# Optimization experiments

Hardware: AMD Instinct MI355X
Metric: run time of the kernel (lower is better)

Reference implementation:

```python
import jax, jax.numpy as jnp
import numpy as np

INPUT_DIM = 400
G_DIM = 3 * INPUT_DIM          # 1200, per-mention repr dim
GIJ_DIM = 9 * INPUT_DIM        # 3600, pair repr dim
HIDDEN = 150
M = 10000                      # candidate mentions
P = 2000                       # pruned mentions


def _pair_positions(P, K):
    """Static (numpy) construction of (i_pos, j_pos) into pruned_idx, matching
    the original double loop: for idx, for j in pruned_idx[max(0, idx-K):idx]."""
    I = np.repeat(np.arange(P)[:, None], K, axis=1)      # [P, K]
    Jpos = I - np.arange(K, 0, -1)[None, :]              # j = idx-K .. idx-1 (ascending)
    valid = Jpos >= 0
    return I[valid], Jpos[valid]                         # row-major => same ordering as loop


def setup_inputs() -> dict:
    key = jax.random.key(0)
    ks = jax.random.split(key, 8)
    mention_reprs = jax.random.normal(ks[0], (M, G_DIM), dtype=jnp.float32)
    pruned_idx = jnp.sort(jax.random.randint(ks[1], (P,), 0, M))
    s = 0.02
    return {
        "mention_reprs": mention_reprs,
        "pruned_idx": pruned_idx,
        "K": 50,
        "W1": jax.random.normal(ks[2], (GIJ_DIM, HIDDEN), dtype=jnp.float32) * s,
        "b1": jnp.zeros((HIDDEN,), dtype=jnp.float32),
        "W2": jax.random.normal(ks[3], (HIDDEN, HIDDEN), dtype=jnp.float32) * s,
        "b2": jnp.zeros((HIDDEN,), dtype=jnp.float32),
        "W3": jax.random.normal(ks[4], (HIDDEN, 1), dtype=jnp.float32) * s,
        "b3": jnp.zeros((1,), dtype=jnp.float32),
    }


def reference(mention_reprs, pruned_idx, K, W1, b1, W2, b2, W3, b3):
    P_ = pruned_idx.shape[0]
    i_pos, j_pos = _pair_positions(P_, int(K))           # static shapes
    g_i = mention_reprs[pruned_idx[i_pos]]               # [NP, G_DIM]
    g_j = mention_reprs[pruned_idx[j_pos]]               # [NP, G_DIM]
    pairwise = jnp.concatenate([g_i, g_j, g_i * g_j], axis=1)  # [NP, 9*input_dim]
    h = jax.nn.relu(pairwise @ W1 + b1)
    h = jax.nn.relu(h @ W2 + b2)
    return (h @ W3 + b3).squeeze(-1)                     # [NP]
```

## Files before the change

kernel.cpp:

```cpp
#include <hip/hip_runtime.h>


typedef __attribute__((ext_vector_type(8))) short short8;
typedef __attribute__((ext_vector_type(4))) float f32x4;

constexpr int DP    = 1216;
constexpr int HPAD  = 160;
constexpr int NKC   = 38;
constexpr int NKC2  = 5;
constexpr int WCHU  = 10240;
constexpr int WCH1  = 5120;
constexpr int ROWS  = 128;
constexpr int KD    = 50;
constexpr int TI    = 5;
constexpr int PB    = TI * KD;
constexpr int NGR   = KD + TI;
constexpr int TD    = KD * (KD - 1) / 2;

__device__ __forceinline__ ushort bf16_rne(float x) {
  uint u = __float_as_uint(x);
  u += 0x7FFFu + ((u >> 16) & 1u);
  return (ushort)(u >> 16);
}
__device__ __forceinline__ float bf16f(ushort h) {
  return __uint_as_float((uint)h << 16);
}
__device__ __forceinline__ f32x4 mfma16(short8 a, short8 b, f32x4 c) {
  return __builtin_amdgcn_mfma_f32_16x16x32_bf16(a, b, c, 0, 0, 0);
}
__device__ __forceinline__ void g2lds16(const void* g, void* l) {
  __builtin_amdgcn_global_load_lds(
      (const __attribute__((address_space(1))) void*)g,
      (__attribute__((address_space(3))) void*)l, 16, 0, 0);
}
__device__ __forceinline__ void stage_hi(const ushort* gs, ushort* lb,
                                         int w, int lane) {
  const char* g = (const char*)gs + w * 1024 + lane * 16;
  char* l = (char*)lb + w * 1024;
  g2lds16(g, l);
  g2lds16(g + 4096, l + 4096);
  if (w < 2) g2lds16(g + 8192, l + 8192);
}
__device__ __forceinline__ void stage_chunk(const ushort* gsrc, ushort* lbuf,
                                            int w, int lane) {
  const char* g = (const char*)gsrc + w * 5120 + lane * 16;
  char* l = (char*)lbuf + w * 5120;
#pragma unroll
  for (int q = 0; q < 5; ++q) g2lds16(g + q * 1024, l + q * 1024);
}
__device__ __forceinline__ void stage_G5(const float* __restrict__ G, int b0,
                                         int c, float* buf, int w, int lane) {
#pragma unroll
  for (int r = 0; r < 2; ++r) {
    const int slot = r * 256 + w * 64 + lane;
    int row = slot >> 3, grp = slot & 7;
    row = min(row, NGR - 1);
    const float* src =
        G + (size_t)(b0 + row) * DP + c * 32 + ((grp ^ (row & 7)) << 2);
    char* dst = (char*)buf + (r * 256 + w * 64) * 16;
    g2lds16(src, dst);
  }
}
__device__ __forceinline__ short8 mulcvt8(float4 a0, float4 a1, float4 b0,
                                          float4 b1) {
  float p[8] = {a0.x * b0.x, a0.y * b0.y, a0.z * b0.z, a0.w * b0.w,
                a1.x * b1.x, a1.y * b1.y, a1.z * b1.z, a1.w * b1.w};
  uint r[4];
#pragma unroll
  for (int e = 0; e < 4; ++e) {
    uint u0 = __float_as_uint(p[2 * e]);
    uint u1 = __float_as_uint(p[2 * e + 1]);
    u0 += 0x7FFFu + ((u0 >> 16) & 1u);
    u1 += 0x7FFFu + ((u1 >> 16) & 1u);
    r[e] = __builtin_amdgcn_perm(u1, u0, 0x07060302u);
  }
  uint4 h = make_uint4(r[0], r[1], r[2], r[3]);
  return *(short8*)&h;
}
__device__ __forceinline__ void split1(const float* a, short8& hi, short8& lo) {
  const float4 a0 = *(const float4*)a, a1 = *(const float4*)(a + 4);
  float p[8] = {a0.x, a0.y, a0.z, a0.w, a1.x, a1.y, a1.z, a1.w};
  uint h[4], l[4];
#pragma unroll
  for (int e = 0; e < 4; ++e) {
    uint u0 = __float_as_uint(p[2 * e]), u1 = __float_as_uint(p[2 * e + 1]);
    float r0 = p[2 * e] - __uint_as_float(u0 & 0xffff0000u);
    float r1 = p[2 * e + 1] - __uint_as_float(u1 & 0xffff0000u);
    h[e] = __builtin_amdgcn_perm(u1, u0, 0x07060302u);
    l[e] = __builtin_amdgcn_perm(__float_as_uint(r1), __float_as_uint(r0),
                                 0x07060302u);
  }
  uint4 hu = make_uint4(h[0], h[1], h[2], h[3]);
  uint4 lu = make_uint4(l[0], l[1], l[2], l[3]);
  hi = *(short8*)&hu; lo = *(short8*)&lu;
}
__device__ __forceinline__ void pair_ij(int r, int K, int NP, int& i, int& j) {
  if (r >= NP) { i = 1; j = 0; return; }
  const int T = K * (K - 1) / 2;
  if (r < T) {
    int ii = (int)((1.0f + sqrtf(1.0f + 8.0f * (float)r)) * 0.5f);
    while (ii * (ii - 1) / 2 > r) --ii;
    while ((ii + 1) * ii / 2 <= r) ++ii;
    i = ii; j = r - ii * (ii - 1) / 2;
  } else {
    const int rp = r - T, q = rp / K;
    i = K + q; j = i - K + (rp - q * K);
  }
}

__global__ void k_prep_gather(const float* __restrict__ W1,
                              const float* __restrict__ W2,
                              const float* __restrict__ M,
                              const int* __restrict__ pidx,
                              ushort* __restrict__ W1ab,
                              ushort* __restrict__ W1c_hi,
                              ushort* __restrict__ W2_hi,
                              float* __restrict__ G, int P) {
  if ((int)blockIdx.x < P) {
    const int i = blockIdx.x;
    const int r = pidx[i];
    const float4* src = reinterpret_cast<const float4*>(M + (size_t)r * 1200);
    float4* dst = reinterpret_cast<float4*>(G + (size_t)i * DP);
    for (int t = threadIdx.x; t < DP / 4; t += blockDim.x)
      dst[t] = (t < 300) ? src[t] : make_float4(0.f, 0.f, 0.f, 0.f);
    return;
  }
  const int NAB = 2 * NKC * HPAD * 32;
  const int NC = NKC * HPAD * 32;
  int idx = (blockIdx.x - P) * 256 + threadIdx.x;
  if (idx < NAB) {
    int s = idx / NC, r1 = idx % NC;
    int c = r1 / (HPAD * 32), r2 = r1 % (HPAD * 32);
    int col = r2 >> 5, kk = r2 & 31;
    int k = c * 32 + kk;
    float v = (k < 1200 && col < 150) ? W1[((size_t)s * 1200 + k) * 150 + col] : 0.f;
    ushort h = bf16_rne(v);
    ushort l = bf16_rne(v - bf16f(h));
    size_t base = (size_t)(s * NKC + c) * WCHU;
    int i0 = (col * 32 + kk) ^ ((col & 7) << 3);
    W1ab[base + i0] = h;
    W1ab[base + i0 + 5120] = l;
  } else if (idx < NAB + NC) {
    int r1 = idx - NAB;
    int c = r1 / (HPAD * 32), r2 = r1 % (HPAD * 32);
    int col = r2 >> 5, kk = r2 & 31;
    int k = c * 32 + kk;
    float v = (k < 1200 && col < 150)
                  ? W1[((size_t)2 * 1200 + k) * 150 + col] : 0.f;
    int i0 = (col * 32 + kk) ^ ((col & 7) << 3);
    W1c_hi[(size_t)c * WCH1 + i0] = bf16_rne(v);
  } else {
    int r1 = idx - NAB - NC;
    if (r1 < NKC2 * HPAD * 32) {
      int c = r1 / (HPAD * 32), r2 = r1 % (HPAD * 32);
      int col = r2 >> 5, kk = r2 & 31;
      int k = c * 32 + kk;
      float v = (k < 150 && col < 150) ? W2[(size_t)k * 150 + col] : 0.f;
      int i0 = (col * 32 + kk) ^ ((col & 7) << 3);
      W2_hi[(size_t)c * WCH1 + i0] = bf16_rne(v);
    }
  }
}

__global__ __launch_bounds__(256, 4) void k_precomp(
    const float* __restrict__ G, const ushort* __restrict__ W1ab,
    const float* __restrict__ b1, float* __restrict__ AB, int P) {
  __shared__ __align__(16) ushort Wb[2][WCHU];
  const int tid = threadIdx.x, lane = tid & 63, w = tid >> 6;
  const int l15 = lane & 15, kb = lane >> 4;
  const int rt = w & 1, ch = w >> 1;
  const int r0 = blockIdx.x * 32;
  const int slab = blockIdx.y;
  const ushort* wsrc = W1ab + (size_t)slab * NKC * WCHU;

  const int row = min(r0 + rt * 16 + l15, P - 1);
  const float* g = G + (size_t)row * DP + kb * 8;
  const int lbase = (l15 * 32 + kb * 8) ^ ((l15 & 7) << 3);

  f32x4 acc[5];
#pragma unroll
  for (int b = 0; b < 5; ++b) acc[b] = (f32x4)(0.f);

  stage_chunk(wsrc, Wb[0], w, lane);
  short8 ah, al;
  split1(g, ah, al);

  for (int c = 0; c < NKC; ++c) {
    __syncthreads();
    if (c < NKC - 1)
      stage_chunk(wsrc + (size_t)(c + 1) * WCHU, Wb[(c + 1) & 1], w, lane);
    const ushort* wb = Wb[c & 1];
#pragma unroll
    for (int ct = 0; ct < 5; ++ct) {
      const int ob = (ch * 5 + ct) * 512 + lbase;
      const short8 bh = *(const short8*)&wb[ob];
      const short8 bl = *(const short8*)&wb[ob + 5120];
      acc[ct] = mfma16(ah, bh, acc[ct]);
      acc[ct] = mfma16(al, bh, acc[ct]);
      acc[ct] = mfma16(ah, bl, acc[ct]);
    }
    if (c < NKC - 1) split1(g + (c + 1) * 32, ah, al);
  }
  float* outp = AB + (size_t)slab * P * HPAD;
#pragma unroll
  for (int q = 0; q < 4; ++q) {
    const int r = r0 + rt * 16 + kb * 4 + q;
    if (r < P) {
#pragma unroll
      for (int ct = 0; ct < 5; ++ct) {
        const int col = (ch * 5 + ct) * 16 + l15;
        float v = acc[ct][q];
        if (slab == 0 && col < 150) v += b1[col];
        outp[(size_t)r * HPAD + col] = v;
      }
    }
  }
}

__global__ __launch_bounds__(256, 2) void k_pair(
    const float* __restrict__ G, const ushort* __restrict__ W1c_hi,
    const float* __restrict__ AB, ushort* __restrict__ H1,
    int P, int K, int NP, int ND, int wmax) {
  __shared__ __align__(16) ushort Wb[2][WCH1];
  __shared__ __align__(16) float Gs[2][2048];
  __shared__ int tI[ROWS], tJ[ROWS];
  const int tid = threadIdx.x, lane = tid & 63, w = tid >> 6;
  const int l15 = lane & 15, kb = lane >> 4;
  const int lswz = (l15 * 32 + kb * 8) ^ ((l15 & 7) << 3);

  if ((int)blockIdx.x < ND) {
    const int q8 = ND >> 3, r8 = ND & 7;
    const int xcd = blockIdx.x & 7, sidx = blockIdx.x >> 3;
    const int bid = (xcd < r8) ? xcd * (q8 + 1) + sidx
                               : r8 * (q8 + 1) + (xcd - r8) * q8 + sidx;
    const int i0 = KD + bid * TI;
    const int b0 = i0 - KD;

    int sI0[4], sI1[4], sJ0[4], sJ1[4];
#pragma unroll
    for (int rt = 0; rt < 4; ++rt) {
      const int q = min(w * 64 + rt * 16 + l15, PB - 1);
      const int li = KD + q / KD, lj = q / KD + q % KD;
      sI0[rt] = li * 8 + ((2 * kb) ^ (li & 7));
      sI1[rt] = li * 8 + ((2 * kb + 1) ^ (li & 7));
      sJ0[rt] = lj * 8 + ((2 * kb) ^ (lj & 7));
      sJ1[rt] = lj * 8 + ((2 * kb + 1) ^ (lj & 7));
    }

    f32x4 acc[4][10];
#pragma unroll
    for (int a = 0; a < 4; ++a)
#pragma unroll
      for (int b = 0; b < 10; ++b) acc[a][b] = (f32x4)(0.f);

    stage_G5(G, b0, 0, Gs[0], w, lane);
    stage_hi(W1c_hi, Wb[0], w, lane);
    __syncthreads();

#pragma unroll 2
    for (int c = 0; c < NKC; ++c) {
      if (c) __syncthreads();
      if (c < NKC - 1) {
        stage_G5(G, b0, c + 1, Gs[(c + 1) & 1], w, lane);
        stage_hi(W1c_hi + (size_t)(c + 1) * WCH1, Wb[(c + 1) & 1], w, lane);
      }
      const float4* gp = (const float4*)Gs[c & 1];
      const ushort* wb = Wb[c & 1];
      short8 a[4];
#pragma unroll
      for (int rt = 0; rt < 4; ++rt)
        a[rt] = mulcvt8(gp[sI0[rt]], gp[sI1[rt]], gp[sJ0[rt]], gp[sJ1[rt]]);
#pragma unroll
      for (int ct = 0; ct < 10; ++ct) {
        const short8 bh = *(const short8*)&wb[ct * 512 + lswz];
        acc[0][ct] = mfma16(a[0], bh, acc[0][ct]);
        acc[1][ct] = mfma16(a[1], bh, acc[1][ct]);
        acc[2][ct] = mfma16(a[2], bh, acc[2][ct]);
        acc[3][ct] = mfma16(a[3], bh, acc[3][ct]);
      }
    }

#pragma unroll
    for (int rt = 0; rt < 4; ++rt)
#pragma unroll
      for (int qq = 0; qq < 4; ++qq) {
        const int rr = w * 64 + rt * 16 + kb * 4 + qq;
        if (rr < PB) {
          const int ii = i0 + rr / KD;
          const int jj = ii - KD + rr % KD;
          const float* Ar = AB + (size_t)ii * HPAD;
          const float* Br = AB + ((size_t)P + jj) * HPAD;
          ushort* hrow = H1 + (size_t)(TD + bid * PB + rr) * HPAD;
#pragma unroll
          for (int ct = 0; ct < 10; ++ct) {
            const int col = ct * 16 + l15;
            const float v = acc[rt][ct][qq] + Ar[col] + Br[col];
            hrow[col] = bf16_rne(fmaxf(v, 0.f));
          }
        }
      }
  } else {
    const int r0 = ((int)blockIdx.x - ND) * ROWS;
    if (tid < ROWS) {
      int i, j;
      pair_ij(r0 + tid, K, NP, i, j);
      tI[tid] = i; tJ[tid] = j;
    }
    stage_hi(W1c_hi, Wb[0], w, lane);
    __syncthreads();

    const int rowA = w * 32 + l15, rowB = rowA + 16;
    const float* gi0 = G + (size_t)tI[rowA] * DP + kb * 8;
    const float* gj0 = G + (size_t)tJ[rowA] * DP + kb * 8;
    const float* gi1 = G + (size_t)tI[rowB] * DP + kb * 8;
    const float* gj1 = G + (size_t)tJ[rowB] * DP + kb * 8;

    f32x4 acc[2][10];
#pragma unroll
    for (int a = 0; a < 2; ++a)
#pragma unroll
      for (int b = 0; b < 10; ++b) acc[a][b] = (f32x4)(0.f);

    float4 x00 = *(const float4*)gi0, x01 = *(const float4*)(gi0 + 4);
    float4 y00 = *(const float4*)gj0, y01 = *(const float4*)(gj0 + 4);
    float4 x10 = *(const float4*)gi1, x11 = *(const float4*)(gi1 + 4);
    float4 y10 = *(const float4*)gj1, y11 = *(const float4*)(gj1 + 4);

#pragma unroll 2
    for (int c = 0; c < NKC; ++c) {
      if (c) __syncthreads();
      if (c < NKC - 1)
        stage_hi(W1c_hi + (size_t)(c + 1) * WCH1, Wb[(c + 1) & 1], w, lane);
      const short8 a0 = mulcvt8(x00, x01, y00, y01);
      const short8 a1 = mulcvt8(x10, x11, y10, y11);
      if (c < NKC - 1) {
        const int cn = c + 1;
        x00 = *(const float4*)(gi0 + cn * 32); x01 = *(const float4*)(gi0 + cn * 32 + 4);
        y00 = *(const float4*)(gj0 + cn * 32); y01 = *(const float4*)(gj0 + cn * 32 + 4);
        x10 = *(const float4*)(gi1 + cn * 32); x11 = *(const float4*)(gi1 + cn * 32 + 4);
        y10 = *(const float4*)(gj1 + cn * 32); y11 = *(const float4*)(gj1 + cn * 32 + 4);
      }
      const ushort* wb = Wb[c & 1];
#pragma unroll
      for (int ct = 0; ct < 10; ++ct) {
        const short8 bh = *(const short8*)&wb[ct * 512 + lswz];
        acc[0][ct] = mfma16(a0, bh, acc[0][ct]);
        acc[1][ct] = mfma16(a1, bh, acc[1][ct]);
      }
    }

#pragma unroll
    for (int rt = 0; rt < 2; ++rt)
#pragma unroll
      for (int q = 0; q < 4; ++q) {
        const int rr = w * 32 + rt * 16 + kb * 4 + q;
        const int gr = r0 + rr;
        if (gr < wmax) {
          const float* Ar = AB + (size_t)tI[rr] * HPAD;
          const float* Br = AB + ((size_t)P + tJ[rr]) * HPAD;
          ushort* hrow = H1 + (size_t)gr * HPAD;
#pragma unroll
          for (int ct = 0; ct < 10; ++ct) {
            const int col = ct * 16 + l15;
            const float v = acc[rt][ct][q] + Ar[col] + Br[col];
            hrow[col] = bf16_rne(fmaxf(v, 0.f));
          }
        }
      }
  }
}

__global__ __launch_bounds__(256, 3) void k_mlp(
    const ushort* __restrict__ H1, const ushort* __restrict__ W2_hi,
    const float* __restrict__ b2, const float* __restrict__ W3,
    const float* __restrict__ b3, float* __restrict__ out, int NP) {
  __shared__ __align__(16) ushort Wb[2][WCH1];
  const int tid = threadIdx.x, lane = tid & 63, w = tid >> 6;
  const int l15 = lane & 15, kb = lane >> 4;
  const int r0 = blockIdx.x * ROWS;
  const int lswz = (l15 * 32 + kb * 8) ^ ((l15 & 7) << 3);

  const ushort* h0 = H1 + (size_t)(r0 + w * 32 + l15) * HPAD + kb * 8;
  const ushort* h1 = H1 + (size_t)(r0 + w * 32 + 16 + l15) * HPAD + kb * 8;

  f32x4 acc[2][10];
#pragma unroll
  for (int a = 0; a < 2; ++a)
#pragma unroll
    for (int b = 0; b < 10; ++b) acc[a][b] = (f32x4)(0.f);

  stage_hi(W2_hi, Wb[0], w, lane);
  short8 a0 = *(const short8*)h0;
  short8 a1 = *(const short8*)h1;

#pragma unroll
  for (int c = 0; c < NKC2; ++c) {
    __syncthreads();
    if (c < NKC2 - 1)
      stage_hi(W2_hi + (size_t)(c + 1) * WCH1, Wb[(c + 1) & 1], w, lane);
    const ushort* wb = Wb[c & 1];
#pragma unroll
    for (int ct = 0; ct < 10; ++ct) {
      const short8 bh = *(const short8*)&wb[ct * 512 + lswz];
      acc[0][ct] = mfma16(a0, bh, acc[0][ct]);
      acc[1][ct] = mfma16(a1, bh, acc[1][ct]);
    }
    if (c < NKC2 - 1) {
      a0 = *(const short8*)(h0 + (c + 1) * 32);
      a1 = *(const short8*)(h1 + (c + 1) * 32);
    }
  }
  const float b3v = b3[0];
#pragma unroll
  for (int rt = 0; rt < 2; ++rt)
#pragma unroll
    for (int q = 0; q < 4; ++q) {
      float s = 0.f;
#pragma unroll
      for (int ct = 0; ct < 10; ++ct) {
        const int col = ct * 16 + l15;
        const float b2c = (col < 150) ? b2[col] : 0.f;
        const float w3c = (col < 150) ? W3[col] : 0.f;
        s = fmaf(fmaxf(acc[rt][ct][q] + b2c, 0.f), w3c, s);
      }
      s += __shfl_xor(s, 1); s += __shfl_xor(s, 2);
      s += __shfl_xor(s, 4); s += __shfl_xor(s, 8);
      if (l15 == 0) {
        const int gr = r0 + w * 32 + rt * 16 + kb * 4 + q;
        if (gr < NP) out[gr] = s + b3v;
      }
    }
}

extern "C" void kernel_launch(void* const* d_in, const int* in_sizes, int n_in,
                              void* d_out, int out_size, void* d_ws, size_t ws_size,
                              hipStream_t stream) {
  const float* M    = (const float*)d_in[0];
  const int*   pidx = (const int*)d_in[1];
  const float* W1   = (const float*)d_in[3];
  const float* b1   = (const float*)d_in[4];
  const float* W2   = (const float*)d_in[5];
  const float* b2   = (const float*)d_in[6];
  const float* W3   = (const float*)d_in[7];
  const float* b3   = (const float*)d_in[8];
  float* out = (float*)d_out;

  const int P = in_sizes[1];
  const int NP = out_size;
  int K = 50;
  for (int k = 1; k <= P; ++k) {
    const long long np = (long long)k * (k - 1) / 2 + (long long)(P - k) * k;
    if (np == (long long)NP) { K = k; break; }
  }
  const int nb = (NP + ROWS - 1) / ROWS;

  float* G = (float*)d_ws;
  float* AB = G + (size_t)P * DP;
  ushort* W1ab = (ushort*)(AB + (size_t)2 * P * HPAD);
  ushort* W1c_hi = W1ab + (size_t)2 * NKC * WCHU;
  ushort* W2_hi = W1c_hi + (size_t)NKC * WCH1;
  ushort* H1 = W2_hi + (size_t)NKC2 * WCH1;

  const int prepN = (2 * NKC + NKC + NKC2) * HPAD * 32;
  const int prepB = (prepN + 255) / 256;
  k_prep_gather<<<P + prepB, 256, 0, stream>>>(W1, W2, M, pidx, W1ab, W1c_hi,
                                               W2_hi, G, P);
  dim3 gp((P + 31) / 32, 2);
  k_precomp<<<gp, 256, 0, stream>>>(G, W1ab, b1, AB, P);

  int ND = 0, wmax = NP;
  if (K == KD && P > KD && (P - KD) % TI == 0) {
    ND = (P - KD) / TI;
    wmax = TD;
  }
  const int genB = (wmax + ROWS - 1) / ROWS;
  k_pair<<<ND + genB, 256, 0, stream>>>(G, W1c_hi, AB, H1, P, K, NP, ND, wmax);
  k_mlp<<<nb, 256, 0, stream>>>(H1, W2_hi, b2, W3, b3, out, NP);
}
```

Measured before the change: 125.9 us.

## Retile pair kernel to 8 anchors per 512-thread block with per-wave i reuse

The dense pair path now handles 8 anchor mentions per block using 8 waves, one per anchor, so each wave loads its g_i row once and reuses it across all 64 j rows. Per-block G staging shrinks to one 16-byte load per thread and W1 staging is split across more waves. The generic fallback path is reorganized into head and tail regions so it can cover pairs left over when P-K is not divisible by 8. The bf16 conversion in the product helper now uses the HIP bf16x2 intrinsic. Doubling the block size raises register pressure under the new launch bounds and may reduce occupancy.

```diff
diff --git a/kernel.cpp b/kernel.cpp
--- a/kernel.cpp
+++ b/kernel.cpp
@@ -1,4 +1,5 @@
 #include <hip/hip_runtime.h>
+#include <hip/hip_bf16.h>
 
 
 typedef __attribute__((ext_vector_type(8))) short short8;
@@ -12,9 +13,8 @@
 constexpr int WCH1  = 5120;
 constexpr int ROWS  = 128;
 constexpr int KD    = 50;
-constexpr int TI    = 5;
-constexpr int PB    = TI * KD;
-constexpr int NGR   = KD + TI;
+constexpr int TI8   = 8;
+constexpr int NGR8  = KD + TI8;
 constexpr int TD    = KD * (KD - 1) / 2;
 
 __device__ __forceinline__ ushort bf16_rne(float x) {
@@ -41,6 +41,13 @@
   g2lds16(g + 4096, l + 4096);
   if (w < 2) g2lds16(g + 8192, l + 8192);
 }
+__device__ __forceinline__ void stage_hi8(const ushort* gs, ushort* lb,
+                                          int w, int lane) {
+  const char* g = (const char*)gs + w * 1024 + lane * 16;
+  char* l = (char*)lb + w * 1024;
+  g2lds16(g, l);
+  if (w < 2) g2lds16(g + 8192, l + 8192);
+}
 __device__ __forceinline__ void stage_chunk(const ushort* gsrc, ushort* lbuf,
                                             int w, int lane) {
   const char* g = (const char*)gsrc + w * 5120 + lane * 16;
@@ -48,18 +55,13 @@
 #pragma unroll
   for (int q = 0; q < 5; ++q) g2lds16(g + q * 1024, l + q * 1024);
 }
-__device__ __forceinline__ void stage_G5(const float* __restrict__ G, int b0,
+__device__ __forceinline__ void stage_G8(const float* __restrict__ G, int b0,
                                          int c, float* buf, int w, int lane) {
-#pragma unroll
-  for (int r = 0; r < 2; ++r) {
-    const int slot = r * 256 + w * 64 + lane;
-    int row = slot >> 3, grp = slot & 7;
-    row = min(row, NGR - 1);
-    const float* src =
-        G + (size_t)(b0 + row) * DP + c * 32 + ((grp ^ (row & 7)) << 2);
-    char* dst = (char*)buf + (r * 256 + w * 64) * 16;
-    g2lds16(src, dst);
-  }
+  const int slot = w * 64 + lane;
+  const int row = min(slot >> 3, NGR8 - 1), grp = slot & 7;
+  const float* src =
+      G + (size_t)(b0 + row) * DP + c * 32 + ((grp ^ (row & 7)) << 2);
+  g2lds16(src, (char*)buf + w * 1024);
 }
 __device__ __forceinline__ short8 mulcvt8(float4 a0, float4 a1, float4 b0,
                                           float4 b1) {
@@ -68,11 +70,8 @@
   uint r[4];
 #pragma unroll
   for (int e = 0; e < 4; ++e) {
-    uint u0 = __float_as_uint(p[2 * e]);
-    uint u1 = __float_as_uint(p[2 * e + 1]);
-    u0 += 0x7FFFu + ((u0 >> 16) & 1u);
-    u1 += 0x7FFFu + ((u1 >> 16) & 1u);
-    r[e] = __builtin_amdgcn_perm(u1, u0, 0x07060302u);
+    __hip_bfloat162 t = __float22bfloat162_rn(make_float2(p[2 * e], p[2 * e + 1]));
+    r[e] = *(uint*)&t;
   }
   uint4 h = make_uint4(r[0], r[1], r[2], r[3]);
   return *(short8*)&h;
@@ -217,13 +216,13 @@
   }
 }
 
-__global__ __launch_bounds__(256, 2) void k_pair(
+__global__ __launch_bounds__(512, 2) void k_pair(
     const float* __restrict__ G, const ushort* __restrict__ W1c_hi,
     const float* __restrict__ AB, ushort* __restrict__ H1,
-    int P, int K, int NP, int ND, int wmax) {
+    int P, int K, int NP, int ND, int headB, int tail0, int wlimHead) {
   __shared__ __align__(16) ushort Wb[2][WCH1];
   __shared__ __align__(16) float Gs[2][2048];
-  __shared__ int tI[ROWS], tJ[ROWS];
+  __shared__ int tI[256], tJ[256];
   const int tid = threadIdx.x, lane = tid & 63, w = tid >> 6;
   const int l15 = lane & 15, kb = lane >> 4;
   const int lswz = (l15 * 32 + kb * 8) ^ ((l15 & 7) << 3);
@@ -233,18 +232,18 @@
     const int xcd = blockIdx.x & 7, sidx = blockIdx.x >> 3;
     const int bid = (xcd < r8) ? xcd * (q8 + 1) + sidx
                                : r8 * (q8 + 1) + (xcd - r8) * q8 + sidx;
-    const int i0 = KD + bid * TI;
+    const int i0 = KD + bid * TI8;
     const int b0 = i0 - KD;
 
-    int sI0[4], sI1[4], sJ0[4], sJ1[4];
+    const int gir = KD + w;
+    const int sI0 = gir * 8 + ((2 * kb) ^ (gir & 7));
+    const int sI1 = gir * 8 + ((2 * kb + 1) ^ (gir & 7));
+    int sJ0[4], sJ1[4];
 #pragma unroll
     for (int rt = 0; rt < 4; ++rt) {
-      const int q = min(w * 64 + rt * 16 + l15, PB - 1);
-      const int li = KD + q / KD, lj = q / KD + q % KD;
-      sI0[rt] = li * 8 + ((2 * kb) ^ (li & 7));
-      sI1[rt] = li * 8 + ((2 * kb + 1) ^ (li & 7));
-      sJ0[rt] = lj * 8 + ((2 * kb) ^ (lj & 7));
-      sJ1[rt] = lj * 8 + ((2 * kb + 1) ^ (lj & 7));
+      const int rj = min(w + rt * 16 + l15, NGR8 - 1);
+      sJ0[rt] = rj * 8 + ((2 * kb) ^ (rj & 7));
+      sJ1[rt] = rj * 8 + ((2 * kb + 1) ^ (rj & 7));
     }
 
     f32x4 acc[4][10];
@@ -253,23 +252,24 @@
 #pragma unroll
       for (int b = 0; b < 10; ++b) acc[a][b] = (f32x4)(0.f);
 
-    stage_G5(G, b0, 0, Gs[0], w, lane);
-    stage_hi(W1c_hi, Wb[0], w, lane);
+    stage_G8(G, b0, 0, Gs[0], w, lane);
+    stage_hi8(W1c_hi, Wb[0], w, lane);
     __syncthreads();
 
 #pragma unroll 2
     for (int c = 0; c < NKC; ++c) {
       if (c) __syncthreads();
       if (c < NKC - 1) {
-        stage_G5(G, b0, c + 1, Gs[(c + 1) & 1], w, lane);
-        stage_hi(W1c_hi + (size_t)(c + 1) * WCH1, Wb[(c + 1) & 1], w, lane);
+        stage_G8(G, b0, c + 1, Gs[(c + 1) & 1], w, lane);
+        stage_hi8(W1c_hi + (size_t)(c + 1) * WCH1, Wb[(c + 1) & 1], w, lane);
       }
       const float4* gp = (const float4*)Gs[c & 1];
       const ushort* wb = Wb[c & 1];
+      const float4 xi0 = gp[sI0], xi1 = gp[sI1];
       short8 a[4];
 #pragma unroll
       for (int rt = 0; rt < 4; ++rt)
-        a[rt] = mulcvt8(gp[sI0[rt]], gp[sI1[rt]], gp[sJ0[rt]], gp[sJ1[rt]]);
+        a[rt] = mulcvt8(xi0, xi1, gp[sJ0[rt]], gp[sJ1[rt]]);
 #pragma unroll
       for (int ct = 0; ct < 10; ++ct) {
         const short8 bh = *(const short8*)&wb[ct * 512 + lswz];
@@ -280,17 +280,17 @@
       }
     }
 
+    const int ii = i0 + w;
+    const float* Ar = AB + (size_t)ii * HPAD;
 #pragma unroll
     for (int rt = 0; rt < 4; ++rt)
 #pragma unroll
       for (int qq = 0; qq < 4; ++qq) {
-        const int rr = w * 64 + rt * 16 + kb * 4 + qq;
-        if (rr < PB) {
-          const int ii = i0 + rr / KD;
-          const int jj = ii - KD + rr % KD;
-          const float* Ar = AB + (size_t)ii * HPAD;
+        const int jloc = rt * 16 + kb * 4 + qq;
+        if (jloc < KD) {
+          const int jj = ii - KD + jloc;
           const float* Br = AB + ((size_t)P + jj) * HPAD;
-          ushort* hrow = H1 + (size_t)(TD + bid * PB + rr) * HPAD;
+          ushort* hrow = H1 + (size_t)(TD + (size_t)(ii - KD) * KD + jloc) * HPAD;
 #pragma unroll
           for (int ct = 0; ct < 10; ++ct) {
             const int col = ct * 16 + l15;
@@ -300,13 +300,15 @@
         }
       }
   } else {
-    const int r0 = ((int)blockIdx.x - ND) * ROWS;
-    if (tid < ROWS) {
+    const int g = (int)blockIdx.x - ND;
+    const int r0 = (g < headB) ? g * 256 : tail0 + (g - headB) * 256;
+    const int wlim = (g < headB) ? wlimHead : NP;
+    if (tid < 256) {
       int i, j;
       pair_ij(r0 + tid, K, NP, i, j);
       tI[tid] = i; tJ[tid] = j;
     }
-    stage_hi(W1c_hi, Wb[0], w, lane);
+    stage_hi8(W1c_hi, Wb[0], w, lane);
     __syncthreads();
 
     const int rowA = w * 32 + l15, rowB = rowA + 16;
@@ -330,7 +332,7 @@
     for (int c = 0; c < NKC; ++c) {
       if (c) __syncthreads();
       if (c < NKC - 1)
-        stage_hi(W1c_hi + (size_t)(c + 1) * WCH1, Wb[(c + 1) & 1], w, lane);
+        stage_hi8(W1c_hi + (size_t)(c + 1) * WCH1, Wb[(c + 1) & 1], w, lane);
       const short8 a0 = mulcvt8(x00, x01, y00, y01);
       const short8 a1 = mulcvt8(x10, x11, y10, y11);
       if (c < NKC - 1) {
@@ -355,7 +357,7 @@
       for (int q = 0; q < 4; ++q) {
         const int rr = w * 32 + rt * 16 + kb * 4 + q;
         const int gr = r0 + rr;
-        if (gr < wmax) {
+        if (gr < wlim) {
           const float* Ar = AB + (size_t)tI[rr] * HPAD;
           const float* Br = AB + ((size_t)P + tJ[rr]) * HPAD;
           ushort* hrow = H1 + (size_t)gr * HPAD;
@@ -468,12 +470,17 @@
   dim3 gp((P + 31) / 32, 2);
   k_precomp<<<gp, 256, 0, stream>>>(G, W1ab, b1, AB, P);
 
-  int ND = 0, wmax = NP;
-  if (K == KD && P > KD && (P - KD) % TI == 0) {
-    ND = (P - KD) / TI;
-    wmax = TD;
-  }
-  const int genB = (wmax + ROWS - 1) / ROWS;
-  k_pair<<<ND + genB, 256, 0, stream>>>(G, W1c_hi, AB, H1, P, K, NP, ND, wmax);
+  int ND = 0, headB, tail0 = NP, wlimHead = NP;
+  if (K == KD && P > KD + TI8) {
+    ND = (P - KD) / TI8;
+    tail0 = TD + ND * TI8 * KD;
+    wlimHead = TD;
+    headB = (TD + 255) / 256;
+  } else {
+    headB = (NP + 255) / 256;
+  }
+  const int tailB = (NP - tail0 + 255) / 256;
+  k_pair<<<ND + headB + tailB, 512, 0, stream>>>(G, W1c_hi, AB, H1, P, K, NP,
+                                                 ND, headB, tail0, wlimHead);
   k_mlp<<<nb, 256, 0, stream>>>(H1, W2_hi, b2, W3, b3, out, NP);
 }
```

New measurement: 131.0 us. 4.0% more time.

## Fuse second MLP layer and output projection into pair kernel epilogue

Applied to the files above, without the earlier changes.

Removes the separate k_mlp kernel and the H1 bf16 intermediate buffer. Each pair block now stages its relu'd layer-1 activations in reused shared memory, runs the 150x150 layer-2 MFMA with W2 read straight from global memory (unswizzled layout), and reduces against W3 to write final outputs. This avoids the H1 global write/read round trip and one kernel launch. In exchange it adds extra barriers, serialises the per-wave staging phases, and loads uncached W2 fragments. It also switches the bf16 conversion to the packed HIP intrinsic.

```diff
diff --git a/kernel.cpp b/kernel.cpp
--- a/kernel.cpp
+++ b/kernel.cpp
@@ -1,4 +1,5 @@
 #include <hip/hip_runtime.h>
+#include <hip/hip_bf16.h>
 
 
 typedef __attribute__((ext_vector_type(8))) short short8;
@@ -10,12 +11,12 @@
 constexpr int NKC2  = 5;
 constexpr int WCHU  = 10240;
 constexpr int WCH1  = 5120;
-constexpr int ROWS  = 128;
 constexpr int KD    = 50;
 constexpr int TI    = 5;
 constexpr int PB    = TI * KD;
 constexpr int NGR   = KD + TI;
 constexpr int TD    = KD * (KD - 1) / 2;
+constexpr int TP    = 168;
 
 __device__ __forceinline__ ushort bf16_rne(float x) {
   uint u = __float_as_uint(x);
@@ -57,8 +58,7 @@
     row = min(row, NGR - 1);
     const float* src =
         G + (size_t)(b0 + row) * DP + c * 32 + ((grp ^ (row & 7)) << 2);
-    char* dst = (char*)buf + (r * 256 + w * 64) * 16;
-    g2lds16(src, dst);
+    g2lds16(src, (char*)buf + (r * 256 + w * 64) * 16);
   }
 }
 __device__ __forceinline__ short8 mulcvt8(float4 a0, float4 a1, float4 b0,
@@ -68,11 +68,8 @@
   uint r[4];
 #pragma unroll
   for (int e = 0; e < 4; ++e) {
-    uint u0 = __float_as_uint(p[2 * e]);
-    uint u1 = __float_as_uint(p[2 * e + 1]);
-    u0 += 0x7FFFu + ((u0 >> 16) & 1u);
-    u1 += 0x7FFFu + ((u1 >> 16) & 1u);
-    r[e] = __builtin_amdgcn_perm(u1, u0, 0x07060302u);
+    __hip_bfloat162 t = __float22bfloat162_rn(make_float2(p[2 * e], p[2 * e + 1]));
+    r[e] = *(uint*)&t;
   }
   uint4 h = make_uint4(r[0], r[1], r[2], r[3]);
   return *(short8*)&h;
@@ -156,8 +153,7 @@
       int col = r2 >> 5, kk = r2 & 31;
       int k = c * 32 + kk;
       float v = (k < 150 && col < 150) ? W2[(size_t)k * 150 + col] : 0.f;
-      int i0 = (col * 32 + kk) ^ ((col & 7) << 3);
-      W2_hi[(size_t)c * WCH1 + i0] = bf16_rne(v);
+      W2_hi[(size_t)c * WCH1 + col * 32 + kk] = bf16_rne(v);
     }
   }
 }
@@ -219,14 +215,23 @@
 
 __global__ __launch_bounds__(256, 2) void k_pair(
     const float* __restrict__ G, const ushort* __restrict__ W1c_hi,
-    const float* __restrict__ AB, ushort* __restrict__ H1,
-    int P, int K, int NP, int ND, int wmax) {
-  __shared__ __align__(16) ushort Wb[2][WCH1];
-  __shared__ __align__(16) float Gs[2][2048];
-  __shared__ int tI[ROWS], tJ[ROWS];
+    const ushort* __restrict__ W2_hi, const float* __restrict__ AB,
+    const float* __restrict__ b2, const float* __restrict__ W3,
+    const float* __restrict__ b3, float* __restrict__ out,
+    int P, int K, int NP, int ND, int wlimHead) {
+  __shared__ __align__(16) char smem[38912];
+  ushort* Wb0 = (ushort*)smem;
+  ushort* Wb1 = (ushort*)(smem + 10240);
+  float*  Gs0 = (float*)(smem + 20480);
+  float*  Gs1 = (float*)(smem + 28672);
+  ushort* T   = (ushort*)smem;
+  int* tI = (int*)(smem + 36864);
+  int* tJ = (int*)(smem + 37888);
+
   const int tid = threadIdx.x, lane = tid & 63, w = tid >> 6;
   const int l15 = lane & 15, kb = lane >> 4;
   const int lswz = (l15 * 32 + kb * 8) ^ ((l15 & 7) << 3);
+  const float* ABB = AB + (size_t)P * HPAD;
 
   if ((int)blockIdx.x < ND) {
     const int q8 = ND >> 3, r8 = ND & 7;
@@ -253,19 +258,19 @@
 #pragma unroll
       for (int b = 0; b < 10; ++b) acc[a][b] = (f32x4)(0.f);
 
-    stage_G5(G, b0, 0, Gs[0], w, lane);
-    stage_hi(W1c_hi, Wb[0], w, lane);
+    stage_G5(G, b0, 0, Gs0, w, lane);
+    stage_hi(W1c_hi, Wb0, w, lane);
     __syncthreads();
 
 #pragma unroll 2
     for (int c = 0; c < NKC; ++c) {
       if (c) __syncthreads();
       if (c < NKC - 1) {
-        stage_G5(G, b0, c + 1, Gs[(c + 1) & 1], w, lane);
-        stage_hi(W1c_hi + (size_t)(c + 1) * WCH1, Wb[(c + 1) & 1], w, lane);
-      }
-      const float4* gp = (const float4*)Gs[c & 1];
-      const ushort* wb = Wb[c & 1];
+        stage_G5(G, b0, c + 1, (c & 1) ? Gs0 : Gs1, w, lane);
+        stage_hi(W1c_hi + (size_t)(c + 1) * WCH1, (c & 1) ? Wb0 : Wb1, w, lane);
+      }
+      const float4* gp = (const float4*)((c & 1) ? Gs1 : Gs0);
+      const ushort* wb = (c & 1) ? Wb1 : Wb0;
       short8 a[4];
 #pragma unroll
       for (int rt = 0; rt < 4; ++rt)
@@ -280,33 +285,78 @@
       }
     }
 
-#pragma unroll
-    for (int rt = 0; rt < 4; ++rt)
+    float b2v[10], w3v[10];
+#pragma unroll
+    for (int ct = 0; ct < 10; ++ct) {
+      const int col = ct * 16 + l15;
+      b2v[ct] = (col < 150) ? b2[col] : 0.f;
+      w3v[ct] = (col < 150) ? W3[col] : 0.f;
+    }
+    const float b3v = b3[0];
+    for (int s = 0; s < 4; ++s) {
+      __syncthreads();
+      if (w == s) {
+#pragma unroll
+        for (int rt = 0; rt < 4; ++rt)
+#pragma unroll
+          for (int qq = 0; qq < 4; ++qq) {
+            const int rr = w * 64 + rt * 16 + kb * 4 + qq;
+            const int lr = rt * 16 + kb * 4 + qq;
+            if (rr < PB) {
+              const int ii = i0 + rr / KD;
+              const int jj = ii - KD + rr % KD;
+              const float* Ar = AB + (size_t)ii * HPAD;
+              const float* Br = ABB + (size_t)jj * HPAD;
+#pragma unroll
+              for (int ct = 0; ct < 10; ++ct) {
+                const int col = ct * 16 + l15;
+                const float v = acc[rt][ct][qq] + Ar[col] + Br[col];
+                T[lr * TP + col] = bf16_rne(fmaxf(v, 0.f));
+              }
+            } else {
+#pragma unroll
+              for (int ct = 0; ct < 10; ++ct) T[lr * TP + ct * 16 + l15] = 0;
+            }
+          }
+      }
+      __syncthreads();
+      f32x4 acc2[10];
+#pragma unroll
+      for (int b = 0; b < 10; ++b) acc2[b] = (f32x4)(0.f);
+#pragma unroll
+      for (int c2 = 0; c2 < NKC2; ++c2) {
+        const short8 a2 =
+            *(const short8*)&T[(w * 16 + l15) * TP + c2 * 32 + kb * 8];
+#pragma unroll
+        for (int ct = 0; ct < 10; ++ct) {
+          const short8 bfr = *(const short8*)&W2_hi[(size_t)c2 * WCH1 +
+                                                    (ct * 16 + l15) * 32 + kb * 8];
+          acc2[ct] = mfma16(a2, bfr, acc2[ct]);
+        }
+      }
 #pragma unroll
       for (int qq = 0; qq < 4; ++qq) {
-        const int rr = w * 64 + rt * 16 + kb * 4 + qq;
-        if (rr < PB) {
-          const int ii = i0 + rr / KD;
-          const int jj = ii - KD + rr % KD;
-          const float* Ar = AB + (size_t)ii * HPAD;
-          const float* Br = AB + ((size_t)P + jj) * HPAD;
-          ushort* hrow = H1 + (size_t)(TD + bid * PB + rr) * HPAD;
-#pragma unroll
-          for (int ct = 0; ct < 10; ++ct) {
-            const int col = ct * 16 + l15;
-            const float v = acc[rt][ct][qq] + Ar[col] + Br[col];
-            hrow[col] = bf16_rne(fmaxf(v, 0.f));
-          }
+        float sum = 0.f;
+#pragma unroll
+        for (int ct = 0; ct < 10; ++ct)
+          sum = fmaf(fmaxf(acc2[ct][qq] + b2v[ct], 0.f), w3v[ct], sum);
+        sum += __shfl_xor(sum, 1); sum += __shfl_xor(sum, 2);
+        sum += __shfl_xor(sum, 4); sum += __shfl_xor(sum, 8);
+        if (l15 == 0) {
+          const int rr = s * 64 + w * 16 + kb * 4 + qq;
+          if (rr < PB) out[TD + (size_t)bid * PB + rr] = sum + b3v;
         }
       }
+    }
   } else {
-    const int r0 = ((int)blockIdx.x - ND) * ROWS;
-    if (tid < ROWS) {
+    const int r0 = ((int)blockIdx.x - ND) * 128;
+    const int wlim = wlimHead;
+    if (tid < 128) {
       int i, j;
       pair_ij(r0 + tid, K, NP, i, j);
       tI[tid] = i; tJ[tid] = j;
     }
-    stage_hi(W1c_hi, Wb[0], w, lane);
+    stage_hi(W1c_hi, Wb0, w, lane);
     __syncthreads();
 
     const int rowA = w * 32 + l15, rowB = rowA + 16;
@@ -330,7 +380,7 @@
     for (int c = 0; c < NKC; ++c) {
       if (c) __syncthreads();
       if (c < NKC - 1)
-        stage_hi(W1c_hi + (size_t)(c + 1) * WCH1, Wb[(c + 1) & 1], w, lane);
+        stage_hi(W1c_hi + (size_t)(c + 1) * WCH1, (c & 1) ? Wb0 : Wb1, w, lane);
       const short8 a0 = mulcvt8(x00, x01, y00, y01);
       const short8 a1 = mulcvt8(x10, x11, y10, y11);
       if (c < NKC - 1) {
@@ -340,7 +390,7 @@
         x10 = *(const float4*)(gi1 + cn * 32); x11 = *(const float4*)(gi1 + cn * 32 + 4);
         y10 = *(const float4*)(gj1 + cn * 32); y11 = *(const float4*)(gj1 + cn * 32 + 4);
       }
-      const ushort* wb = Wb[c & 1];
+      const ushort* wb = (c & 1) ? Wb1 : Wb0;
 #pragma unroll
       for (int ct = 0; ct < 10; ++ct) {
         const short8 bh = *(const short8*)&wb[ct * 512 + lswz];
@@ -349,87 +399,63 @@
       }
     }
 
-#pragma unroll
-    for (int rt = 0; rt < 2; ++rt)
-#pragma unroll
-      for (int q = 0; q < 4; ++q) {
-        const int rr = w * 32 + rt * 16 + kb * 4 + q;
-        const int gr = r0 + rr;
-        if (gr < wmax) {
-          const float* Ar = AB + (size_t)tI[rr] * HPAD;
-          const float* Br = AB + ((size_t)P + tJ[rr]) * HPAD;
-          ushort* hrow = H1 + (size_t)gr * HPAD;
-#pragma unroll
-          for (int ct = 0; ct < 10; ++ct) {
-            const int col = ct * 16 + l15;
-            const float v = acc[rt][ct][q] + Ar[col] + Br[col];
-            hrow[col] = bf16_rne(fmaxf(v, 0.f));
+    float b2v[10], w3v[10];
+#pragma unroll
+    for (int ct = 0; ct < 10; ++ct) {
+      const int col = ct * 16 + l15;
+      b2v[ct] = (col < 150) ? b2[col] : 0.f;
+      w3v[ct] = (col < 150) ? W3[col] : 0.f;
+    }
+    const float b3v = b3[0];
+    for (int s = 0; s < 2; ++s) {
+      __syncthreads();
+      if ((w >> 1) == s) {
+#pragma unroll
+        for (int rt = 0; rt < 2; ++rt)
+#pragma unroll
+          for (int qq = 0; qq < 4; ++qq) {
+            const int rr = w * 32 + rt * 16 + kb * 4 + qq;
+            const int lr = (w & 1) * 32 + rt * 16 + kb * 4 + qq;
+            const float* Ar = AB + (size_t)tI[rr] * HPAD;
+            const float* Br = ABB + (size_t)tJ[rr] * HPAD;
+#pragma unroll
+            for (int ct = 0; ct < 10; ++ct) {
+              const int col = ct * 16 + l15;
+              const float v = acc[rt][ct][qq] + Ar[col] + Br[col];
+              T[lr * TP + col] = bf16_rne(fmaxf(v, 0.f));
+            }
           }
+      }
+      __syncthreads();
+      f32x4 acc2[10];
+#pragma unroll
+      for (int b = 0; b < 10; ++b) acc2[b] = (f32x4)(0.f);
+#pragma unroll
+      for (int c2 = 0; c2 < NKC2; ++c2) {
+        const short8 a2 =
+            *(const short8*)&T[(w * 16 + l15) * TP + c2 * 32 + kb * 8];
+#pragma unroll
+        for (int ct = 0; ct < 10; ++ct) {
+          const short8 bfr = *(const short8*)&W2_hi[(size_t)c2 * WCH1 +
+                                                    (ct * 16 + l15) * 32 + kb * 8];
+          acc2[ct] = mfma16(a2, bfr, acc2[ct]);
         }
       }
-  }
-}
-
-__global__ __launch_bounds__(256, 3) void k_mlp(
-    const ushort* __restrict__ H1, const ushort* __restrict__ W2_hi,
-    const float* __restrict__ b2, const float* __restrict__ W3,
-    const float* __restrict__ b3, float* __restrict__ out, int NP) {
-  __shared__ __align__(16) ushort Wb[2][WCH1];
-  const int tid = threadIdx.x, lane = tid & 63, w = tid >> 6;
-  const int l15 = lane & 15, kb = lane >> 4;
-  const int r0 = blockIdx.x * ROWS;
-  const int lswz = (l15 * 32 + kb * 8) ^ ((l15 & 7) << 3);
-
-  const ushort* h0 = H1 + (size_t)(r0 + w * 32 + l15) * HPAD + kb * 8;
-  const ushort* h1 = H1 + (size_t)(r0 + w * 32 + 16 + l15) * HPAD + kb * 8;
-
-  f32x4 acc[2][10];
-#pragma unroll
-  for (int a = 0; a < 2; ++a)
-#pragma unroll
-    for (int b = 0; b < 10; ++b) acc[a][b] = (f32x4)(0.f);
-
-  stage_hi(W2_hi, Wb[0], w, lane);
-  short8 a0 = *(const short8*)h0;
-  short8 a1 = *(const short8*)h1;
-
-#pragma unroll
-  for (int c = 0; c < NKC2; ++c) {
-    __syncthreads();
-    if (c < NKC2 - 1)
-      stage_hi(W2_hi + (size_t)(c + 1) * WCH1, Wb[(c + 1) & 1], w, lane);
-    const ushort* wb = Wb[c & 1];
-#pragma unroll
-    for (int ct = 0; ct < 10; ++ct) {
-      const short8 bh = *(const short8*)&wb[ct * 512 + lswz];
-      acc[0][ct] = mfma16(a0, bh, acc[0][ct]);
-      acc[1][ct] = mfma16(a1, bh, acc[1][ct]);
-    }
-    if (c < NKC2 - 1) {
-      a0 = *(const short8*)(h0 + (c + 1) * 32);
-      a1 = *(const short8*)(h1 + (c + 1) * 32);
-    }
-  }
-  const float b3v = b3[0];
-#pragma unroll
-  for (int rt = 0; rt < 2; ++rt)
-#pragma unroll
-    for (int q = 0; q < 4; ++q) {
-      float s = 0.f;
-#pragma unroll
-      for (int ct = 0; ct < 10; ++ct) {
-        const int col = ct * 16 + l15;
-        const float b2c = (col < 150) ? b2[col] : 0.f;
-        const float w3c = (col < 150) ? W3[col] : 0.f;
-        s = fmaf(fmaxf(acc[rt][ct][q] + b2c, 0.f), w3c, s);
-      }
-      s += __shfl_xor(s, 1); s += __shfl_xor(s, 2);
-      s += __shfl_xor(s, 4); s += __shfl_xor(s, 8);
-      if (l15 == 0) {
-        const int gr = r0 + w * 32 + rt * 16 + kb * 4 + q;
-        if (gr < NP) out[gr] = s + b3v;
-      }
-    }
+#pragma unroll
+      for (int qq = 0; qq < 4; ++qq) {
+        float sum = 0.f;
+#pragma unroll
+        for (int ct = 0; ct < 10; ++ct)
+          sum = fmaf(fmaxf(acc2[ct][qq] + b2v[ct], 0.f), w3v[ct], sum);
+        sum += __shfl_xor(sum, 1); sum += __shfl_xor(sum, 2);
+        sum += __shfl_xor(sum, 4); sum += __shfl_xor(sum, 8);
+        if (l15 == 0) {
+          const int gr = r0 + s * 64 + w * 16 + kb * 4 + qq;
+          if (gr < wlim) out[gr] = sum + b3v;
+        }
+      }
+    }
+  }
 }
 
 extern "C" void kernel_launch(void* const* d_in, const int* in_sizes, int n_in,
@@ -452,14 +478,12 @@
     const long long np = (long long)k * (k - 1) / 2 + (long long)(P - k) * k;
     if (np == (long long)NP) { K = k; break; }
   }
-  const int nb = (NP + ROWS - 1) / ROWS;
 
   float* G = (float*)d_ws;
   float* AB = G + (size_t)P * DP;
   ushort* W1ab = (ushort*)(AB + (size_t)2 * P * HPAD);
   ushort* W1c_hi = W1ab + (size_t)2 * NKC * WCHU;
   ushort* W2_hi = W1c_hi + (size_t)NKC * WCH1;
-  ushort* H1 = W2_hi + (size_t)NKC2 * WCH1;
 
   const int prepN = (2 * NKC + NKC + NKC2) * HPAD * 32;
   const int prepB = (prepN + 255) / 256;
@@ -468,12 +492,15 @@
   dim3 gp((P + 31) / 32, 2);
   k_precomp<<<gp, 256, 0, stream>>>(G, W1ab, b1, AB, P);
 
-  int ND = 0, wmax = NP;
+  int ND = 0, wlimHead, headB;
   if (K == KD && P > KD && (P - KD) % TI == 0) {
     ND = (P - KD) / TI;
-    wmax = TD;
-  }
-  const int genB = (wmax + ROWS - 1) / ROWS;
-  k_pair<<<ND + genB, 256, 0, stream>>>(G, W1c_hi, AB, H1, P, K, NP, ND, wmax);
-  k_mlp<<<nb, 256, 0, stream>>>(H1, W2_hi, b2, W3, b3, out, NP);
-}
+    wlimHead = TD;
+    headB = (TD + 127) / 128;
+  } else {
+    wlimHead = NP;
+    headB = (NP + 127) / 128;
+  }
+  k_pair<<<ND + headB, 256, 0, stream>>>(G, W1c_hi, W2_hi, AB, b2, W3, b3, out,
+                                         P, K, NP, ND, wlimHead);
+}
```

Result: slower. 328.1 us (+160.5%).
